# Performance work log

Measured on AMD Instinct MI355X. Metric: run time of the kernel, lower is better.

## Reference

```python
import jax, jax.numpy as jnp
import numpy as np
import math

HIDDEN = 768
HEADS = 12
HEAD_DIM = HIDDEN // HEADS
B, N = 128, 196
POS = 196


def setup_inputs() -> dict:
    key = jax.random.key(0)
    ks = jax.random.split(key, 12)
    s = 1.0 / math.sqrt(HIDDEN)
    inp = {
        "x": jax.random.normal(ks[0], (B, N, HIDDEN), dtype=jnp.float32),
        "Wq": jax.random.normal(ks[1], (HIDDEN, HIDDEN), dtype=jnp.float32) * s,
        "bq": jnp.zeros((HIDDEN,), dtype=jnp.float32),
        "Wk": jax.random.normal(ks[2], (HIDDEN, HIDDEN), dtype=jnp.float32) * s,
        "bk": jnp.zeros((HIDDEN,), dtype=jnp.float32),
        "Wv": jax.random.normal(ks[3], (HIDDEN, HIDDEN), dtype=jnp.float32) * s,
        "bv": jnp.zeros((HIDDEN,), dtype=jnp.float32),
        "Wp": jax.random.normal(ks[4], (HIDDEN, HIDDEN), dtype=jnp.float32) * s,
        "bp": jnp.zeros((HIDDEN,), dtype=jnp.float32),
        "pos_bias": jax.random.normal(ks[5], (POS, POS), dtype=jnp.float32) * 0.02,
        "mask": jnp.ones((B, 1, 1, N), dtype=jnp.int32),
    }
    return inp


def reference(x, Wq, bq, Wk, bk, Wv, bv, Wp, bp, pos_bias, mask):
    Bx, Nx, C = x.shape
    H, D = HEADS, HEAD_DIM
    # nn.Linear: y = x @ W.T + b
    q = (x @ Wq.T + bq).reshape(Bx, Nx, H, D).transpose(0, 2, 1, 3)  # [B,H,N,D]
    k = (x @ Wk.T + bk).reshape(Bx, Nx, H, D).transpose(0, 2, 1, 3)
    v = (x @ Wv.T + bv).reshape(Bx, Nx, H, D).transpose(0, 2, 1, 3)
    attn = jnp.einsum('bhnd,bhmd->bhnm', q, k) / math.sqrt(D)
    attn = attn + pos_bias[:Nx, :Nx][None, None, :, :]
    attn = jnp.where(mask == 0, -jnp.inf, attn)
    attn = jax.nn.softmax(attn, axis=-1)
    out = jnp.einsum('bhnm,bhmd->bhnd', attn, v)
    out = out.transpose(0, 2, 1, 3).reshape(Bx, Nx, C)
    return out @ Wp.T + bp
```

## Files before the change

### kernel.cpp

```cpp
#include <hip/hip_runtime.h>
#include <hip/hip_bf16.h>

#define HIDDEN 768
#define HEADS 12
#define HEAD_DIM 64
#define BATCH 128
#define SEQ 196
#define M_TOT (BATCH * SEQ)
#define QKV_N (3 * HIDDEN)

typedef __attribute__((ext_vector_type(8))) short bf16x8;
typedef __attribute__((ext_vector_type(8))) unsigned short u16x8;
typedef __attribute__((ext_vector_type(4))) float f32x4;

__device__ __forceinline__ unsigned short f2bf(float f) {
    unsigned int u = __builtin_bit_cast(unsigned int, f);
    unsigned int r = (u + 0x7fffu + ((u >> 16) & 1u)) >> 16;
    return (unsigned short)r;
}

__device__ __forceinline__ ushort4 cvt4(float4 v) {
    ushort4 o;
    o.x = f2bf(v.x); o.y = f2bf(v.y); o.z = f2bf(v.z); o.w = f2bf(v.w);
    return o;
}

__global__ __launch_bounds__(256) void prep_kernel(
    const float* __restrict__ x,
    const float* __restrict__ Wq, const float* __restrict__ Wk,
    const float* __restrict__ Wv, const float* __restrict__ Wp,
    const float* __restrict__ bq, const float* __restrict__ bk,
    const float* __restrict__ bv,
    unsigned short* __restrict__ xb, unsigned short* __restrict__ wqkv,
    unsigned short* __restrict__ wpb, float* __restrict__ biasq)
{
    const long long NX = (long long)M_TOT * HIDDEN / 4;
    const long long NQ = NX + (long long)QKV_N * HIDDEN / 4;
    const long long NP = NQ + (long long)HIDDEN * HIDDEN / 4;
    const long long NB = NP + QKV_N / 4;
    long long tid = (long long)blockIdx.x * 256 + threadIdx.x;
    if (tid < NX) {
        float4 v = ((const float4*)x)[tid];
        ((ushort4*)xb)[tid] = cvt4(v);
    } else if (tid < NQ) {
        int i = (int)(tid - NX);
        int e = i * 4;
        int row = e / HIDDEN, col = e % HIDDEN;
        const float* s = (row < HIDDEN) ? (Wq + (size_t)row * HIDDEN + col)
                       : (row < 2 * HIDDEN) ? (Wk + (size_t)(row - HIDDEN) * HIDDEN + col)
                       : (Wv + (size_t)(row - 2 * HIDDEN) * HIDDEN + col);
        ((ushort4*)wqkv)[i] = cvt4(*(const float4*)s);
    } else if (tid < NP) {
        int i = (int)(tid - NQ);
        ((ushort4*)wpb)[i] = cvt4(((const float4*)Wp)[i]);
    } else if (tid < NB) {
        int i = (int)(tid - NP);
        int e = i * 4;
        const float* s = (e < HIDDEN) ? (bq + e)
                       : (e < 2 * HIDDEN) ? (bk + (e - HIDDEN))
                       : (bv + (e - 2 * HIDDEN));
        *(float4*)(biasq + e) = *(const float4*)s;
    }
}

template <bool OUT_BF16>
__global__ __launch_bounds__(256) void gemm_bt(
    const unsigned short* __restrict__ A,
    const unsigned short* __restrict__ B,
    const float* __restrict__ bias,
    void* __restrict__ C, const int Ncols)
{
    constexpr int K = HIDDEN;
    __shared__ __align__(16) unsigned short As[128 * 32];
    __shared__ __align__(16) unsigned short Bs[128 * 32];
    __shared__ __align__(16) float Cs[4][16][68];
    const int t = threadIdx.x, w = t >> 6, lane = t & 63;
    const int m0 = blockIdx.y * 128, n0 = blockIdx.x * 128;
    const int wm = w >> 1, wn = w & 1;
    const int srow = lane >> 2, scol = (lane & 3) * 8;
    f32x4 acc[4][4] = {};
    const unsigned short* ag0 = A + (size_t)(m0 + w * 16 + srow) * K + scol;
    const unsigned short* bg0 = B + (size_t)(n0 + w * 16 + srow) * K + scol;
    const int l15 = lane & 15, q8 = (lane >> 4) * 8;

    for (int k0 = 0; k0 < K; k0 += 32) {
#pragma unroll
        for (int it = 0; it < 2; ++it) {
            __builtin_amdgcn_global_load_lds(
                (__attribute__((address_space(1))) void*)(ag0 + (size_t)it * 64 * K + k0),
                (__attribute__((address_space(3))) void*)(As + it * 2048 + w * 512),
                16, 0, 0);
            __builtin_amdgcn_global_load_lds(
                (__attribute__((address_space(1))) void*)(bg0 + (size_t)it * 64 * K + k0),
                (__attribute__((address_space(3))) void*)(Bs + it * 2048 + w * 512),
                16, 0, 0);
        }
        __syncthreads();
        bf16x8 af[4], bfv[4];
#pragma unroll
        for (int i = 0; i < 4; ++i) {
            af[i]  = *(const bf16x8*)(As + (wm * 64 + i * 16 + l15) * 32 + q8);
            bfv[i] = *(const bf16x8*)(Bs + (wn * 64 + i * 16 + l15) * 32 + q8);
        }
#pragma unroll
        for (int i = 0; i < 4; ++i)
#pragma unroll
            for (int j = 0; j < 4; ++j)
                acc[i][j] = __builtin_amdgcn_mfma_f32_16x16x32_bf16(af[i], bfv[j], acc[i][j], 0, 0, 0);
        __syncthreads();
    }

    const int quad = lane >> 4;
    float bvj[4];
#pragma unroll
    for (int j = 0; j < 4; ++j) bvj[j] = bias[n0 + wn * 64 + j * 16 + l15];

#pragma unroll
    for (int i = 0; i < 4; ++i) {
        __syncthreads();
#pragma unroll
        for (int j = 0; j < 4; ++j)
#pragma unroll
            for (int r = 0; r < 4; ++r)
                Cs[w][quad * 4 + r][j * 16 + l15] = acc[i][j][r] + bvj[j];
        __syncthreads();
        if constexpr (OUT_BF16) {
#pragma unroll
            for (int p = 0; p < 2; ++p) {
                const int row = p * 8 + (lane >> 3);
                const int c0 = (lane & 7) * 8;
                float4 a = *(const float4*)&Cs[w][row][c0];
                float4 bb = *(const float4*)&Cs[w][row][c0 + 4];
                u16x8 pk;
                pk[0] = f2bf(a.x); pk[1] = f2bf(a.y); pk[2] = f2bf(a.z); pk[3] = f2bf(a.w);
                pk[4] = f2bf(bb.x); pk[5] = f2bf(bb.y); pk[6] = f2bf(bb.z); pk[7] = f2bf(bb.w);
                *(u16x8*)((unsigned short*)C +
                          (size_t)(m0 + wm * 64 + i * 16 + row) * Ncols + n0 + wn * 64 + c0) = pk;
            }
        } else {
#pragma unroll
            for (int p = 0; p < 4; ++p) {
                const int row = p * 4 + (lane >> 4);
                const int c0 = (lane & 15) * 4;
                float4 a = *(const float4*)&Cs[w][row][c0];
                *(float4*)((float*)C +
                           (size_t)(m0 + wm * 64 + i * 16 + row) * Ncols + n0 + wn * 64 + c0) = a;
            }
        }
    }
}

__global__ __launch_bounds__(256, 2) void attn_kernel(
    const unsigned short* __restrict__ QKV,
    const float* __restrict__ pos_bias,
    const int* __restrict__ mask,
    unsigned short* __restrict__ ctx)
{
    __shared__ __align__(16) unsigned short Ks[208 * 72];
    __shared__ __align__(16) unsigned short Vt[64 * 256];
    __shared__ __align__(16) unsigned short Os[4][16 * 72];
    const int b = blockIdx.x / HEADS, h = blockIdx.x % HEADS;
    const int t = threadIdx.x, w = t >> 6, lane = t & 63;
    const int quad = lane >> 4, l15 = lane & 15;
    const size_t base = (size_t)b * SEQ * QKV_N + h * HEAD_DIM;

    for (int c = t; c < SEQ * 8; c += 256) {
        int row = c >> 3, d0 = (c & 7) * 8;
        *(bf16x8*)(Ks + row * 72 + d0) =
            *(const bf16x8*)(QKV + base + (size_t)row * QKV_N + HIDDEN + d0);
    }
    {
        bf16x8 z = {};
        for (int i = t; i < 12 * 9; i += 256) {
            int row = 196 + i / 9, d0 = (i % 9) * 8;
            *(bf16x8*)(Ks + row * 72 + d0) = z;
        }
    }
    for (int i = t; i < 64 * 60; i += 256) {
        int row = i / 60, key = 196 + i % 60;
        int s = (row & 7) ^ ((row >> 3) & 7);
        Vt[row * 256 + ((((key >> 3) ^ s) << 3) | (key & 7))] = 0;
    }
    for (int c = t; c < SEQ * 8; c += 256) {
        int key = c >> 3, d0 = (c & 7) * 8;
        bf16x8 vv = *(const bf16x8*)(QKV + base + (size_t)key * QKV_N + 2 * HIDDEN + d0);
        int cb = key >> 3, kk = key & 7;
#pragma unroll
        for (int j = 0; j < 8; ++j) {
            int row = d0 + j;
            int s = (row & 7) ^ ((row >> 3) & 7);
            Vt[row * 256 + (((cb ^ s) << 3) | kk)] = (unsigned short)vv[j];
        }
    }
    __syncthreads();

    int vs[4];
#pragma unroll
    for (int nt = 0; nt < 4; ++nt) {
        int rr = nt * 16 + l15;
        vs[nt] = (rr & 7) ^ ((rr >> 3) & 7);
    }

    for (int t16 = w; t16 < 13; t16 += 4) {
        const int qrow = min(t16 * 16 + l15, SEQ - 1);
        const unsigned short* qp = QKV + base + (size_t)qrow * QKV_N + quad * 8;
        bf16x8 qf0 = *(const bf16x8*)(qp);
        bf16x8 qf1 = *(const bf16x8*)(qp + 32);

        f32x4 accT[13];
#pragma unroll
        for (int jt = 0; jt < 13; ++jt) {
            const unsigned short* kp = Ks + (jt * 16 + l15) * 72 + quad * 8;
            bf16x8 kf0 = *(const bf16x8*)(kp);
            bf16x8 kf1 = *(const bf16x8*)(kp + 32);
            f32x4 z = {};
            z = __builtin_amdgcn_mfma_f32_16x16x32_bf16(kf0, qf0, z, 0, 0, 0);
            z = __builtin_amdgcn_mfma_f32_16x16x32_bf16(kf1, qf1, z, 0, 0, 0);
            accT[jt] = z;
        }

        float mx = -3e38f;
#pragma unroll
        for (int jt = 0; jt < 13; ++jt) {
            const int key0 = jt * 16 + quad * 4;
            const int kb = min(key0, SEQ - 4);
            float4 pb = *(const float4*)(pos_bias + (size_t)qrow * SEQ + kb);
            int4 mk = *(const int4*)(mask + b * SEQ + kb);
#pragma unroll
            for (int r = 0; r < 4; ++r) {
                const int key = key0 + r;
                const bool cv = (key < SEQ) && ((&mk.x)[r] != 0);
                float v = cv ? (accT[jt][r] * 0.125f + (&pb.x)[r]) : -1e30f;
                accT[jt][r] = v;
                mx = fmaxf(mx, v);
            }
        }
        mx = fmaxf(mx, __shfl_xor(mx, 16, 64));
        mx = fmaxf(mx, __shfl_xor(mx, 32, 64));
        float sm = 0.f;
#pragma unroll
        for (int jt = 0; jt < 13; ++jt)
#pragma unroll
            for (int r = 0; r < 4; ++r) {
                float e = __expf(accT[jt][r] - mx);
                accT[jt][r] = e;
                sm += e;
            }
        sm += __shfl_xor(sm, 16, 64);
        sm += __shfl_xor(sm, 32, 64);
        const float inv = 1.0f / sm;

        unsigned int pk[14][2];
#pragma unroll
        for (int jt = 0; jt < 13; ++jt)
#pragma unroll
            for (int pp = 0; pp < 2; ++pp) {
                unsigned int lo = f2bf(accT[jt][2 * pp] * inv);
                unsigned int hi = f2bf(accT[jt][2 * pp + 1] * inv);
                pk[jt][pp] = (hi << 16) | lo;
            }
        pk[13][0] = 0; pk[13][1] = 0;

        f32x4 o[4] = {};
        const int hi_half = quad >> 1;
        const int sq0 = (quad & 1) * 2 * 16 + l15;
        const int sq1 = sq0 + 16;
#pragma unroll
        for (int kt = 0; kt < 7; ++kt) {
            union { unsigned int u[4]; bf16x8 v; } pf;
#pragma unroll
            for (int u = 0; u < 4; ++u) {
                const int src = (u < 2) ? sq0 : sq1;
                unsigned int a0 = (unsigned int)__shfl((int)pk[2 * kt][u & 1], src, 64);
                unsigned int a1 = (unsigned int)__shfl((int)pk[2 * kt + 1][u & 1], src, 64);
                pf.u[u] = hi_half ? a1 : a0;
            }
#pragma unroll
            for (int nt = 0; nt < 4; ++nt) {
                const int rr = nt * 16 + l15;
                const bf16x8 vf = *(const bf16x8*)(
                    &Vt[rr * 256 + (((kt * 4 + quad) ^ vs[nt]) << 3)]);
                o[nt] = __builtin_amdgcn_mfma_f32_16x16x32_bf16(pf.v, vf, o[nt], 0, 0, 0);
            }
        }

        __builtin_amdgcn_sched_barrier(0);
#pragma unroll
        for (int nt = 0; nt < 4; ++nt)
#pragma unroll
            for (int r = 0; r < 4; ++r)
                Os[w][(quad * 4 + r) * 72 + nt * 16 + l15] = f2bf(o[nt][r]);
        __builtin_amdgcn_sched_barrier(0);
        asm volatile("s_waitcnt lgkmcnt(0)" ::: "memory");
#pragma unroll
        for (int p = 0; p < 2; ++p) {
            const int row = p * 8 + (lane >> 3);
            const int grow = t16 * 16 + row;
            const int c0 = (lane & 7) * 8;
            bf16x8 ov = *(const bf16x8*)&Os[w][row * 72 + c0];
            if (grow < SEQ)
                *(bf16x8*)(ctx + ((size_t)b * SEQ + grow) * HIDDEN + h * HEAD_DIM + c0) = ov;
        }
        __builtin_amdgcn_sched_barrier(0);
    }
}

extern "C" void kernel_launch(void* const* d_in, const int* in_sizes, int n_in,
                              void* d_out, int out_size, void* d_ws, size_t ws_size,
                              hipStream_t stream) {
    const float* x    = (const float*)d_in[0];
    const float* Wq   = (const float*)d_in[1];
    const float* bq   = (const float*)d_in[2];
    const float* Wk   = (const float*)d_in[3];
    const float* bk   = (const float*)d_in[4];
    const float* Wv   = (const float*)d_in[5];
    const float* bv   = (const float*)d_in[6];
    const float* Wp   = (const float*)d_in[7];
    const float* bp   = (const float*)d_in[8];
    const float* pos  = (const float*)d_in[9];
    const int*   mask = (const int*)d_in[10];

    char* ws = (char*)d_ws;
    size_t off = 0;
    auto alloc = [&](size_t bytes) -> char* {
        char* p = ws + off;
        off += (bytes + 255) & ~(size_t)255;
        return p;
    };
    unsigned short* xb    = (unsigned short*)alloc((size_t)M_TOT * HIDDEN * 2);
    unsigned short* wqkv  = (unsigned short*)alloc((size_t)QKV_N * HIDDEN * 2);
    unsigned short* wpb   = (unsigned short*)alloc((size_t)HIDDEN * HIDDEN * 2);
    float*          biasq = (float*)alloc((size_t)QKV_N * 4);
    unsigned short* qkv   = (unsigned short*)alloc((size_t)M_TOT * QKV_N * 2);
    unsigned short* ctx   = (unsigned short*)alloc((size_t)M_TOT * HIDDEN * 2);

    prep_kernel<<<21123, 256, 0, stream>>>(x, Wq, Wk, Wv, Wp, bq, bk, bv,
                                           xb, wqkv, wpb, biasq);
    gemm_bt<true><<<dim3(QKV_N / 128, M_TOT / 128), 256, 0, stream>>>(
        xb, wqkv, biasq, (void*)qkv, QKV_N);
    attn_kernel<<<BATCH * HEADS, 256, 0, stream>>>(qkv, pos, mask, ctx);
    gemm_bt<false><<<dim3(HIDDEN / 128, M_TOT / 128), 256, 0, stream>>>(
        ctx, wpb, bp, d_out, HIDDEN);
}
```

Baseline: 404.5 us.

## Replace GEMMs with 256x256-tile double-buffered swizzled-LDS pipelined kernel

Both projection GEMMs move from a 128x128 tile, 4-wave kernel with single-buffered LDS and a barrier after each k-step to a 256x256 tile, 8-wave kernel. The new kernel uses a 64-wide k-step, XOR-swizzled LDS layout, double buffering with prefetch interleaved into the MFMA phases, s_setprio around MFMAs, and XCD-aware workgroup remapping. The goal is more reuse per byte loaded, hidden global-load latency, and fewer LDS bank conflicts. The costs are far fewer workgroups (M_TOT=25088 divides by 256 evenly; the output GEMM has only 3 column tiles), a large LDS footprint, and fragile manual waitcnt accounting.

```diff
diff --git a/kernel.cpp b/kernel.cpp
--- a/kernel.cpp
+++ b/kernel.cpp
@@ -64,89 +64,147 @@
 }
 
 template <bool OUT_BF16>
-__global__ __launch_bounds__(256) void gemm_bt(
+__global__ __launch_bounds__(512, 2) void gemm256(
     const unsigned short* __restrict__ A,
     const unsigned short* __restrict__ B,
     const float* __restrict__ bias,
     void* __restrict__ C, const int Ncols)
 {
-    constexpr int K = HIDDEN;
-    __shared__ __align__(16) unsigned short As[128 * 32];
-    __shared__ __align__(16) unsigned short Bs[128 * 32];
-    __shared__ __align__(16) float Cs[4][16][68];
+    __shared__ __align__(16) unsigned short SMEM[65536];
     const int t = threadIdx.x, w = t >> 6, lane = t & 63;
-    const int m0 = blockIdx.y * 128, n0 = blockIdx.x * 128;
-    const int wm = w >> 1, wn = w & 1;
-    const int srow = lane >> 2, scol = (lane & 3) * 8;
-    f32x4 acc[4][4] = {};
-    const unsigned short* ag0 = A + (size_t)(m0 + w * 16 + srow) * K + scol;
-    const unsigned short* bg0 = B + (size_t)(n0 + w * 16 + srow) * K + scol;
-    const int l15 = lane & 15, q8 = (lane >> 4) * 8;
-
-    for (int k0 = 0; k0 < K; k0 += 32) {
-#pragma unroll
-        for (int it = 0; it < 2; ++it) {
-            __builtin_amdgcn_global_load_lds(
-                (__attribute__((address_space(1))) void*)(ag0 + (size_t)it * 64 * K + k0),
-                (__attribute__((address_space(3))) void*)(As + it * 2048 + w * 512),
-                16, 0, 0);
-            __builtin_amdgcn_global_load_lds(
-                (__attribute__((address_space(1))) void*)(bg0 + (size_t)it * 64 * K + k0),
-                (__attribute__((address_space(3))) void*)(Bs + it * 2048 + w * 512),
-                16, 0, 0);
-        }
-        __syncthreads();
-        bf16x8 af[4], bfv[4];
-#pragma unroll
-        for (int i = 0; i < 4; ++i) {
-            af[i]  = *(const bf16x8*)(As + (wm * 64 + i * 16 + l15) * 32 + q8);
-            bfv[i] = *(const bf16x8*)(Bs + (wn * 64 + i * 16 + l15) * 32 + q8);
-        }
-#pragma unroll
-        for (int i = 0; i < 4; ++i)
-#pragma unroll
-            for (int j = 0; j < 4; ++j)
-                acc[i][j] = __builtin_amdgcn_mfma_f32_16x16x32_bf16(af[i], bfv[j], acc[i][j], 0, 0, 0);
-        __syncthreads();
-    }
-
-    const int quad = lane >> 4;
+    const int quad = lane >> 4, l15 = lane & 15;
+    const int wm = w >> 2, wn = w & 3;
+
+    const int gx = gridDim.x;
+    const int nwg = gx * (int)gridDim.y;
+    const int orig = blockIdx.y * gx + blockIdx.x;
+    const int qq = nwg >> 3, rr = nwg & 7;
+    const int xcd = orig & 7, loc = orig >> 3;
+    const int wg = (xcd < rr ? xcd * (qq + 1) : rr * (qq + 1) + (xcd - rr) * qq) + loc;
+    const int m0 = (wg / gx) * 256, n0 = (wg % gx) * 256;
+
+    const int row64 = t >> 3, slot = t & 7;
+    const int ksw = (slot ^ (row64 & 7)) << 3;
+    const unsigned short* Ag = A + (size_t)m0 * HIDDEN + ksw;
+    const unsigned short* Bg = B + (size_t)n0 * HIDDEN + ksw;
+    const int ldsw = (w << 3) * 64;
+
+#define STAGEA(bb, tt, pp)                                                          \
+    __builtin_amdgcn_global_load_lds(                                               \
+        (__attribute__((address_space(1))) void*)(Ag + (size_t)((pp) * 64 + row64) * HIDDEN + (tt) * 64), \
+        (__attribute__((address_space(3))) void*)(SMEM + (bb) * 16384 + (pp) * 4096 + ldsw), 16, 0, 0)
+#define STAGEB(bb, tt, pp)                                                          \
+    __builtin_amdgcn_global_load_lds(                                               \
+        (__attribute__((address_space(1))) void*)(Bg + (size_t)((pp) * 64 + row64) * HIDDEN + (tt) * 64), \
+        (__attribute__((address_space(3))) void*)(SMEM + 32768 + (bb) * 16384 + (pp) * 4096 + ldsw), 16, 0, 0)
+
+    const int sw = l15 & 7;
+    const int s0 = (quad ^ sw) << 3;
+    const int s1 = ((quad + 4) ^ sw) << 3;
+    const unsigned short* pa = SMEM + (wm * 128 + l15) * 64;
+    const unsigned short* pb = SMEM + 32768 + (wn * 64 + l15) * 64;
+
+    f32x4 acc[8][4] = {};
+
+#pragma unroll
+    for (int p = 0; p < 4; ++p) STAGEA(0, 0, p);
+#pragma unroll
+    for (int p = 0; p < 4; ++p) STAGEB(0, 0, p);
+#pragma unroll
+    for (int p = 0; p < 4; ++p) STAGEB(1, 1, p);
+    asm volatile("s_waitcnt vmcnt(4)" ::: "memory");
+    __builtin_amdgcn_s_barrier();
+
+#pragma unroll 2
+    for (int kt = 0; kt < 12; ++kt) {
+        const int b = kt & 1;
+        const unsigned short* pab = pa + b * 16384;
+        const unsigned short* pbb = pb + b * 16384;
+        bf16x8 Bf[4][2];
+        bf16x8 Af[2][2];
+
+#pragma unroll
+        for (int ph = 0; ph < 4; ++ph) {
+            const int ib = ph * 2;
+            if (ph == 0) {
+#pragma unroll
+                for (int j = 0; j < 4; ++j) {
+                    Bf[j][0] = *(const bf16x8*)(pbb + j * 1024 + s0);
+                    Bf[j][1] = *(const bf16x8*)(pbb + j * 1024 + s1);
+                }
+            }
+            Af[0][0] = *(const bf16x8*)(pab + ib * 1024 + s0);
+            Af[0][1] = *(const bf16x8*)(pab + ib * 1024 + s1);
+            Af[1][0] = *(const bf16x8*)(pab + ib * 1024 + 1024 + s0);
+            Af[1][1] = *(const bf16x8*)(pab + ib * 1024 + 1024 + s1);
+            if (ph == 0 && kt < 11) { STAGEA(b ^ 1, kt + 1, 0); STAGEA(b ^ 1, kt + 1, 1); }
+            if (ph == 1 && kt < 11) { STAGEA(b ^ 1, kt + 1, 2); STAGEA(b ^ 1, kt + 1, 3); }
+            if (ph == 2 && kt < 10) { STAGEB(b, kt + 2, 0); STAGEB(b, kt + 2, 1); }
+            if (ph == 3 && kt < 10) { STAGEB(b, kt + 2, 2); STAGEB(b, kt + 2, 3); }
+            __builtin_amdgcn_s_barrier();
+            asm volatile("s_waitcnt lgkmcnt(0)" ::: "memory");
+            __builtin_amdgcn_sched_barrier(0);
+            __builtin_amdgcn_s_setprio(1);
+#pragma unroll
+            for (int i = 0; i < 2; ++i)
+#pragma unroll
+                for (int j = 0; j < 4; ++j) {
+                    acc[ib + i][j] = __builtin_amdgcn_mfma_f32_16x16x32_bf16(
+                        Af[i][0], Bf[j][0], acc[ib + i][j], 0, 0, 0);
+                    acc[ib + i][j] = __builtin_amdgcn_mfma_f32_16x16x32_bf16(
+                        Af[i][1], Bf[j][1], acc[ib + i][j], 0, 0, 0);
+                }
+            __builtin_amdgcn_s_setprio(0);
+            if (ph == 3) {
+                if (kt < 10) { asm volatile("s_waitcnt vmcnt(4)" ::: "memory"); }
+                else if (kt == 10) { asm volatile("s_waitcnt vmcnt(0)" ::: "memory"); }
+            }
+            __builtin_amdgcn_s_barrier();
+        }
+    }
+#undef STAGEA
+#undef STAGEB
+
+    __syncthreads();
+    float* Cs = (float*)SMEM + w * (16 * 68);
     float bvj[4];
 #pragma unroll
     for (int j = 0; j < 4; ++j) bvj[j] = bias[n0 + wn * 64 + j * 16 + l15];
 
 #pragma unroll
-    for (int i = 0; i < 4; ++i) {
-        __syncthreads();
+    for (int i = 0; i < 8; ++i) {
+        __builtin_amdgcn_sched_barrier(0);
 #pragma unroll
         for (int j = 0; j < 4; ++j)
 #pragma unroll
             for (int r = 0; r < 4; ++r)
-                Cs[w][quad * 4 + r][j * 16 + l15] = acc[i][j][r] + bvj[j];
-        __syncthreads();
+                Cs[(quad * 4 + r) * 68 + j * 16 + l15] = acc[i][j][r] + bvj[j];
+        __builtin_amdgcn_sched_barrier(0);
+        asm volatile("s_waitcnt lgkmcnt(0)" ::: "memory");
         if constexpr (OUT_BF16) {
 #pragma unroll
             for (int p = 0; p < 2; ++p) {
                 const int row = p * 8 + (lane >> 3);
                 const int c0 = (lane & 7) * 8;
-                float4 a = *(const float4*)&Cs[w][row][c0];
-                float4 bb = *(const float4*)&Cs[w][row][c0 + 4];
+                float4 a = *(const float4*)&Cs[row * 68 + c0];
+                float4 bb = *(const float4*)&Cs[row * 68 + c0 + 4];
                 u16x8 pk;
                 pk[0] = f2bf(a.x); pk[1] = f2bf(a.y); pk[2] = f2bf(a.z); pk[3] = f2bf(a.w);
                 pk[4] = f2bf(bb.x); pk[5] = f2bf(bb.y); pk[6] = f2bf(bb.z); pk[7] = f2bf(bb.w);
                 *(u16x8*)((unsigned short*)C +
-                          (size_t)(m0 + wm * 64 + i * 16 + row) * Ncols + n0 + wn * 64 + c0) = pk;
+                          (size_t)(m0 + wm * 128 + i * 16 + row) * Ncols + n0 + wn * 64 + c0) = pk;
             }
         } else {
 #pragma unroll
             for (int p = 0; p < 4; ++p) {
                 const int row = p * 4 + (lane >> 4);
                 const int c0 = (lane & 15) * 4;
-                float4 a = *(const float4*)&Cs[w][row][c0];
+                float4 a = *(const float4*)&Cs[row * 68 + c0];
                 *(float4*)((float*)C +
-                           (size_t)(m0 + wm * 64 + i * 16 + row) * Ncols + n0 + wn * 64 + c0) = a;
-            }
-        }
+                           (size_t)(m0 + wm * 128 + i * 16 + row) * Ncols + n0 + wn * 64 + c0) = a;
+            }
+        }
+        __builtin_amdgcn_sched_barrier(0);
     }
 }
 
@@ -336,9 +394,9 @@
 
     prep_kernel<<<21123, 256, 0, stream>>>(x, Wq, Wk, Wv, Wp, bq, bk, bv,
                                            xb, wqkv, wpb, biasq);
-    gemm_bt<true><<<dim3(QKV_N / 128, M_TOT / 128), 256, 0, stream>>>(
+    gemm256<true><<<dim3(QKV_N / 256, M_TOT / 256), 512, 0, stream>>>(
         xb, wqkv, biasq, (void*)qkv, QKV_N);
     attn_kernel<<<BATCH * HEADS, 256, 0, stream>>>(qkv, pos, mask, ctx);
-    gemm_bt<false><<<dim3(HIDDEN / 128, M_TOT / 128), 256, 0, stream>>>(
+    gemm256<false><<<dim3(HIDDEN / 256, M_TOT / 256), 512, 0, stream>>>(
         ctx, wpb, bp, d_out, HIDDEN);
 }
```

After: 377.2 us. 1.07x faster.

## Rewrite GEMM with triple-buffered LDS pipeline, swizzle, 128x256 tiles, XCD remap

Applied to the files above, without the earlier changes.

Replaces the single-buffered 128x128 GEMM with a 512-thread 128x256-tile kernel. It prefetches K-tiles two steps ahead into a three-stage LDS ring, using manual vmcnt waits and one barrier per iteration. LDS reads are XOR-swizzled to avoid bank conflicts, and workgroup IDs are remapped so neighbouring tiles share an XCD for L2 reuse. The goal is to hide global-load latency and cut barrier stalls, at the cost of more LDS per block and fragile hand-written wait counts.

```diff
diff --git a/kernel.cpp b/kernel.cpp
--- a/kernel.cpp
+++ b/kernel.cpp
@@ -64,73 +64,109 @@
 }
 
 template <bool OUT_BF16>
-__global__ __launch_bounds__(256) void gemm_bt(
+__global__ __launch_bounds__(512, 4) void gemm_v4(
     const unsigned short* __restrict__ A,
     const unsigned short* __restrict__ B,
     const float* __restrict__ bias,
     void* __restrict__ C, const int Ncols)
 {
-    constexpr int K = HIDDEN;
-    __shared__ __align__(16) unsigned short As[128 * 32];
-    __shared__ __align__(16) unsigned short Bs[128 * 32];
-    __shared__ __align__(16) float Cs[4][16][68];
+    __shared__ __align__(16) unsigned short SMEM[36864];
     const int t = threadIdx.x, w = t >> 6, lane = t & 63;
-    const int m0 = blockIdx.y * 128, n0 = blockIdx.x * 128;
-    const int wm = w >> 1, wn = w & 1;
-    const int srow = lane >> 2, scol = (lane & 3) * 8;
+    const int quad = lane >> 4, l15 = lane & 15;
+    const int wm = w >> 2, wn = w & 3;
+
+    const int gx = gridDim.x;
+    const int nwg = gx * (int)gridDim.y;
+    const int orig = blockIdx.y * gx + blockIdx.x;
+    const int qq = nwg >> 3, rr2 = nwg & 7;
+    const int xcd = orig & 7, loc = orig >> 3;
+    const int wg = (xcd < rr2 ? xcd * (qq + 1) : rr2 * (qq + 1) + (xcd - rr2) * qq) + loc;
+    const int m0 = (wg / gx) * 128, n0 = (wg % gx) * 256;
+
+    const int srow = t >> 2, sslot = t & 3;
+    const int ksw = (sslot ^ (srow & 3)) << 3;
+    const unsigned short* Ag = A + (size_t)(m0 + srow) * HIDDEN + ksw;
+    const unsigned short* Bg = B + (size_t)(n0 + srow) * HIDDEN + ksw;
+    const int aw = w * 512;
+    const int bw = 12288 + w * 512;
+
+#define STAGE(kt2)  do {                                                            \
+    __builtin_amdgcn_global_load_lds(                                               \
+        (__attribute__((address_space(1))) void*)(Ag + (kt2) * 32),                 \
+        (__attribute__((address_space(3))) void*)(SMEM + ((kt2) % 3) * 4096 + aw),  \
+        16, 0, 0);                                                                  \
+    __builtin_amdgcn_global_load_lds(                                               \
+        (__attribute__((address_space(1))) void*)(Bg + (kt2) * 32),                 \
+        (__attribute__((address_space(3))) void*)(SMEM + 12288 + ((kt2) % 3) * 8192 + w * 512), \
+        16, 0, 0);                                                                  \
+    __builtin_amdgcn_global_load_lds(                                               \
+        (__attribute__((address_space(1))) void*)(Bg + (size_t)128 * HIDDEN + (kt2) * 32), \
+        (__attribute__((address_space(3))) void*)(SMEM + 12288 + ((kt2) % 3) * 8192 + 4096 + w * 512), \
+        16, 0, 0);                                                                  \
+  } while (0)
+
+    const int fsw = (quad ^ (l15 & 3)) << 3;
+    const int aoff = (wm * 64 + l15) * 32 + fsw;
+    const int boff = 12288 + (wn * 64 + l15) * 32 + fsw;
+
     f32x4 acc[4][4] = {};
-    const unsigned short* ag0 = A + (size_t)(m0 + w * 16 + srow) * K + scol;
-    const unsigned short* bg0 = B + (size_t)(n0 + w * 16 + srow) * K + scol;
-    const int l15 = lane & 15, q8 = (lane >> 4) * 8;
-
-    for (int k0 = 0; k0 < K; k0 += 32) {
-#pragma unroll
-        for (int it = 0; it < 2; ++it) {
-            __builtin_amdgcn_global_load_lds(
-                (__attribute__((address_space(1))) void*)(ag0 + (size_t)it * 64 * K + k0),
-                (__attribute__((address_space(3))) void*)(As + it * 2048 + w * 512),
-                16, 0, 0);
-            __builtin_amdgcn_global_load_lds(
-                (__attribute__((address_space(1))) void*)(bg0 + (size_t)it * 64 * K + k0),
-                (__attribute__((address_space(3))) void*)(Bs + it * 2048 + w * 512),
-                16, 0, 0);
-        }
-        __syncthreads();
-        bf16x8 af[4], bfv[4];
-#pragma unroll
-        for (int i = 0; i < 4; ++i) {
-            af[i]  = *(const bf16x8*)(As + (wm * 64 + i * 16 + l15) * 32 + q8);
-            bfv[i] = *(const bf16x8*)(Bs + (wn * 64 + i * 16 + l15) * 32 + q8);
-        }
+
+    STAGE(0);
+    STAGE(1);
+    asm volatile("s_waitcnt vmcnt(3)" ::: "memory");
+    __builtin_amdgcn_s_barrier();
+
+#pragma unroll
+    for (int kt = 0; kt < 24; ++kt) {
+        const int bufA = (kt % 3) * 4096, bufB = (kt % 3) * 8192;
+        if (kt < 22) STAGE(kt + 2);
+        bf16x8 Af[4], Bf[4];
 #pragma unroll
         for (int i = 0; i < 4; ++i)
+            Af[i] = *(const bf16x8*)(SMEM + bufA + aoff + i * 512);
+#pragma unroll
+        for (int j = 0; j < 4; ++j)
+            Bf[j] = *(const bf16x8*)(SMEM + bufB + boff + j * 512);
+        asm volatile("s_waitcnt lgkmcnt(0)" ::: "memory");
+        __builtin_amdgcn_sched_barrier(0);
+        __builtin_amdgcn_s_setprio(1);
+#pragma unroll
+        for (int i = 0; i < 4; ++i)
 #pragma unroll
             for (int j = 0; j < 4; ++j)
-                acc[i][j] = __builtin_amdgcn_mfma_f32_16x16x32_bf16(af[i], bfv[j], acc[i][j], 0, 0, 0);
-        __syncthreads();
-    }
-
-    const int quad = lane >> 4;
+                acc[i][j] = __builtin_amdgcn_mfma_f32_16x16x32_bf16(
+                    Af[i], Bf[j], acc[i][j], 0, 0, 0);
+        __builtin_amdgcn_s_setprio(0);
+        __builtin_amdgcn_sched_barrier(0);
+        if (kt < 22)       { asm volatile("s_waitcnt vmcnt(3)" ::: "memory"); }
+        else if (kt == 22) { asm volatile("s_waitcnt vmcnt(0)" ::: "memory"); }
+        if (kt < 23) __builtin_amdgcn_s_barrier();
+    }
+#undef STAGE
+
+    __syncthreads();
+    float* Cs = (float*)SMEM + w * (16 * 68);
     float bvj[4];
 #pragma unroll
     for (int j = 0; j < 4; ++j) bvj[j] = bias[n0 + wn * 64 + j * 16 + l15];
 
 #pragma unroll
     for (int i = 0; i < 4; ++i) {
-        __syncthreads();
+        __builtin_amdgcn_sched_barrier(0);
 #pragma unroll
         for (int j = 0; j < 4; ++j)
 #pragma unroll
             for (int r = 0; r < 4; ++r)
-                Cs[w][quad * 4 + r][j * 16 + l15] = acc[i][j][r] + bvj[j];
-        __syncthreads();
+                Cs[(quad * 4 + r) * 68 + j * 16 + l15] = acc[i][j][r] + bvj[j];
+        __builtin_amdgcn_sched_barrier(0);
+        asm volatile("s_waitcnt lgkmcnt(0)" ::: "memory");
         if constexpr (OUT_BF16) {
 #pragma unroll
             for (int p = 0; p < 2; ++p) {
                 const int row = p * 8 + (lane >> 3);
                 const int c0 = (lane & 7) * 8;
-                float4 a = *(const float4*)&Cs[w][row][c0];
-                float4 bb = *(const float4*)&Cs[w][row][c0 + 4];
+                float4 a = *(const float4*)&Cs[row * 68 + c0];
+                float4 bb = *(const float4*)&Cs[row * 68 + c0 + 4];
                 u16x8 pk;
                 pk[0] = f2bf(a.x); pk[1] = f2bf(a.y); pk[2] = f2bf(a.z); pk[3] = f2bf(a.w);
                 pk[4] = f2bf(bb.x); pk[5] = f2bf(bb.y); pk[6] = f2bf(bb.z); pk[7] = f2bf(bb.w);
@@ -142,11 +178,12 @@
             for (int p = 0; p < 4; ++p) {
                 const int row = p * 4 + (lane >> 4);
                 const int c0 = (lane & 15) * 4;
-                float4 a = *(const float4*)&Cs[w][row][c0];
+                float4 a = *(const float4*)&Cs[row * 68 + c0];
                 *(float4*)((float*)C +
                            (size_t)(m0 + wm * 64 + i * 16 + row) * Ncols + n0 + wn * 64 + c0) = a;
             }
         }
+        __builtin_amdgcn_sched_barrier(0);
     }
 }
 
@@ -336,9 +373,9 @@
 
     prep_kernel<<<21123, 256, 0, stream>>>(x, Wq, Wk, Wv, Wp, bq, bk, bv,
                                            xb, wqkv, wpb, biasq);
-    gemm_bt<true><<<dim3(QKV_N / 128, M_TOT / 128), 256, 0, stream>>>(
+    gemm_v4<true><<<dim3(QKV_N / 256, M_TOT / 128), 512, 0, stream>>>(
         xb, wqkv, biasq, (void*)qkv, QKV_N);
     attn_kernel<<<BATCH * HEADS, 256, 0, stream>>>(qkv, pos, mask, ctx);
-    gemm_bt<false><<<dim3(HIDDEN / 128, M_TOT / 128), 256, 0, stream>>>(
+    gemm_v4<false><<<dim3(HIDDEN / 256, M_TOT / 128), 512, 0, stream>>>(
         ctx, wpb, bp, d_out, HIDDEN);
 }
```

Result: faster. 363.4 us (-10.2%).
